# Kernel optimization log

Measured on AMD Instinct MI355X. Metric: run time of the kernel, lower is better.

Reference implementation:

```python
import jax, jax.numpy as jnp
import numpy as np
import math

B, S, HID = 2, 2048, 512
NH, NKV, HD = 8, 2, 256
ROT = 64          # partial_rotary_factor 0.25 * head_dim 256
ROPE_THETA = 10000000.0
EPS = 1e-6


def _rms_norm(x, w):
    # zero-centered RMSNorm: x / rms * (1 + w)
    rms = jnp.sqrt(jnp.mean(x * x, axis=-1, keepdims=True) + EPS)
    return x / rms * (1.0 + w)


def _partial_rope(x, cos, sin):
    # x: [B,S,H,HD]; cos/sin: [S, ROT//2]
    xr = x[..., :ROT].reshape(*x.shape[:-1], ROT // 2, 2)
    a, b = xr[..., 0], xr[..., 1]
    c = cos[None, :, None, :]
    s = sin[None, :, None, :]
    rot = jnp.stack([a * c - b * s, a * s + b * c], axis=-1).reshape(*x.shape[:-1], ROT)
    return jnp.concatenate([rot, x[..., ROT:]], axis=-1)


def setup_inputs() -> dict:
    key = jax.random.key(0)
    ks = jax.random.split(key, 6)
    x = jax.random.normal(ks[0], (B, S, HID), dtype=jnp.float32)
    # real RoPE frequencies
    inv_freq = 1.0 / (ROPE_THETA ** (np.arange(0, ROT, 2, dtype=np.float32) / ROT))
    t = np.arange(S, dtype=np.float32)
    angles = np.outer(t, inv_freq)  # [S, ROT//2]
    cos = jnp.asarray(np.cos(angles), dtype=jnp.float32)
    sin = jnp.asarray(np.sin(angles), dtype=jnp.float32)
    # additive causal mask [S,S]
    mask = jnp.where(jnp.tril(jnp.ones((S, S), dtype=bool)), 0.0, -1e9).astype(jnp.float32)
    sc = 0.02
    wq = jax.random.normal(ks[1], (HID, NH * HD), dtype=jnp.float32) * sc
    wk = jax.random.normal(ks[2], (HID, NKV * HD), dtype=jnp.float32) * sc
    wv = jax.random.normal(ks[3], (HID, NKV * HD), dtype=jnp.float32) * sc
    wo = jax.random.normal(ks[4], (NH * HD, HID), dtype=jnp.float32) * sc
    q_norm_w = jnp.zeros((HD,), dtype=jnp.float32)
    k_norm_w = jnp.zeros((HD,), dtype=jnp.float32)
    return {"x": x, "cos": cos, "sin": sin, "mask": mask,
            "wq": wq, "wk": wk, "wv": wv, "wo": wo,
            "q_norm_w": q_norm_w, "k_norm_w": k_norm_w}


def reference(x, cos, sin, mask, wq, wk, wv, wo, q_norm_w, k_norm_w):
    b, s, _ = x.shape
    groups = NH // NKV
    q = (x @ wq).reshape(b, s, NH, HD)
    k = (x @ wk).reshape(b, s, NKV, HD)
    v = (x @ wv).reshape(b, s, NKV, HD)
    q = _partial_rope(_rms_norm(q, q_norm_w), cos, sin)
    k = _partial_rope(_rms_norm(k, k_norm_w), cos, sin)
    # GQA: broadcast kv heads to NH
    k = jnp.repeat(k, groups, axis=2)  # [b,s,NH,HD]
    v = jnp.repeat(v, groups, axis=2)
    scale = math.sqrt(HD)
    scores = jnp.einsum('bqhd,bkhd->bhqk', q, k) / scale
    scores = scores + mask[None, None, :, :]
    attn = jax.nn.softmax(scores, axis=-1)
    out = jnp.einsum('bhqk,bkhd->bqhd', attn, v).reshape(b, s, NH * HD)
    return out @ wo
```

## Files before the change

kernel.cpp:

```cpp
#include <hip/hip_runtime.h>

#define S_LEN 2048
#define NHQ 8
#define NKV 2
#define HD 256
#define KVB 32

typedef __attribute__((ext_vector_type(8))) short bf16x8;
typedef __attribute__((ext_vector_type(4))) short bf16x4;
typedef __attribute__((ext_vector_type(4))) float f32x4;
typedef __attribute__((ext_vector_type(16))) float f32x16;
typedef __attribute__((ext_vector_type(4))) unsigned u32x4;

__device__ __forceinline__ short f2bf(float f) {
    unsigned u = __builtin_bit_cast(unsigned, f);
    u += 0x7FFFu + ((u >> 16) & 1u);
    return (short)(u >> 16);
}
__device__ __forceinline__ float bf2f(short s) {
    unsigned u = ((unsigned)(unsigned short)s) << 16;
    return __builtin_bit_cast(float, u);
}
__device__ __forceinline__ unsigned cvtpk(float a, float b) {
    unsigned r;
    asm("v_cvt_pk_bf16_f32 %0, %1, %2" : "=v"(r) : "v"(a), "v"(b));
    return r;
}
__device__ __forceinline__ void gload16(const short* g, short* l) {
    __builtin_amdgcn_global_load_lds((const __attribute__((address_space(1))) unsigned*)g,
                                     (__attribute__((address_space(3))) unsigned*)l, 16, 0, 0);
}
__device__ __forceinline__ float bperm(int srclane, float v) {
    return __builtin_bit_cast(float,
        __builtin_amdgcn_ds_bpermute(srclane * 4, __builtin_bit_cast(int, v)));
}

__global__ __launch_bounds__(256) void cvt_kernel(const float* __restrict__ in,
                                                  short* __restrict__ out, int n) {
    int i = (blockIdx.x * 256 + threadIdx.x) * 4;
    if (i + 3 < n) {
        float4 f = *(const float4*)(in + i);
        bf16x4 o;
        o[0] = f2bf(f.x); o[1] = f2bf(f.y); o[2] = f2bf(f.z); o[3] = f2bf(f.w);
        *(bf16x4*)(out + i) = o;
    }
}

__global__ __launch_bounds__(256) void wt_kernel(const float* __restrict__ in,
                                                 short* __restrict__ out,
                                                 int K, int N) {
    __shared__ short tile[64][72];
    int n0 = blockIdx.x * 64, k0 = blockIdx.y * 64;
    int t = threadIdx.x;
    #pragma unroll
    for (int i = 0; i < 16; i++) {
        int flat = i * 256 + t; int r = flat >> 6, c = flat & 63;
        tile[r][c] = f2bf(in[(long)(k0 + r) * N + n0 + c]);
    }
    __syncthreads();
    #pragma unroll
    for (int i = 0; i < 16; i++) {
        int flat = i * 256 + t; int r = flat >> 6, c = flat & 63;
        out[(long)(n0 + r) * K + k0 + c] = tile[c][r];
    }
}

template<int BN, int WRITE_BF16>
__global__ __launch_bounds__(256) void gemm_bt(const short* __restrict__ A,
                                               const short* __restrict__ Bt,
                                               void* __restrict__ Cv,
                                               int M, int N, int K) {
    constexpr int NI = BN / 32;
    __shared__ short As[128 * 32];
    __shared__ short Bs[BN * 32];
    const int t = threadIdx.x;
    const int lane = t & 63, w = t >> 6;
    const int lr = lane & 15, lg = lane >> 4;
    const int m0 = blockIdx.y * 128, n0 = blockIdx.x * BN;
    const int wm = (w >> 1) * 64, wn = (w & 1) * (BN / 2);

    f32x4 acc[4][NI];
    #pragma unroll
    for (int i = 0; i < 4; i++)
        #pragma unroll
        for (int j = 0; j < NI; j++) acc[i][j] = (f32x4){0.f, 0.f, 0.f, 0.f};

    for (int k0 = 0; k0 < K; k0 += 32) {
        __syncthreads();
        #pragma unroll
        for (int r = 0; r < 2; r++) {
            int sbase = r * 2048 + w * 512;
            int srow = (sbase + lane * 8) >> 5, scol = (sbase + lane * 8) & 31;
            gload16(A + (long)(m0 + srow) * K + k0 + scol, &As[sbase]);
        }
        #pragma unroll
        for (int r = 0; r < BN / 64; r++) {
            int sbase = r * 2048 + w * 512;
            int srow = (sbase + lane * 8) >> 5, scol = (sbase + lane * 8) & 31;
            gload16(Bt + (long)(n0 + srow) * K + k0 + scol, &Bs[sbase]);
        }
        __syncthreads();
        bf16x8 af[4], bfr[NI];
        #pragma unroll
        for (int mi = 0; mi < 4; mi++)
            af[mi] = *(const bf16x8*)&As[(wm + mi * 16 + lr) * 32 + lg * 8];
        #pragma unroll
        for (int ni = 0; ni < NI; ni++)
            bfr[ni] = *(const bf16x8*)&Bs[(wn + ni * 16 + lr) * 32 + lg * 8];
        #pragma unroll
        for (int mi = 0; mi < 4; mi++)
            #pragma unroll
            for (int ni = 0; ni < NI; ni++)
                acc[mi][ni] = __builtin_amdgcn_mfma_f32_16x16x32_bf16(af[mi], bfr[ni], acc[mi][ni], 0, 0, 0);
    }
    #pragma unroll
    for (int mi = 0; mi < 4; mi++)
    #pragma unroll
    for (int ni = 0; ni < NI; ni++)
    #pragma unroll
    for (int r = 0; r < 4; r++) {
        long row = m0 + wm + mi * 16 + lg * 4 + r;
        long col = n0 + wn + ni * 16 + lr;
        float v = acc[mi][ni][r];
        if (WRITE_BF16) ((short*)Cv)[row * N + col] = f2bf(v);
        else            ((float*)Cv)[row * N + col] = v;
    }
}

__global__ __launch_bounds__(256) void norm_rope_kernel(
    const short* __restrict__ in, short* __restrict__ out,
    const float* __restrict__ w, const float* __restrict__ cosb,
    const float* __restrict__ sinb, int H, long ldin, long cofs,
    long ob, long oh, long os, float scale) {
    int vec = blockIdx.x * 4 + (threadIdx.x >> 6);
    int lane = threadIdx.x & 63;
    int token = vec / H, head = vec % H;
    int b = token / S_LEN, s = token % S_LEN;

    bf16x4 xv = *(const bf16x4*)(in + (long)token * ldin + cofs + head * 256 + lane * 4);
    float x0 = bf2f(xv[0]), x1 = bf2f(xv[1]), x2 = bf2f(xv[2]), x3 = bf2f(xv[3]);
    float ss = x0 * x0 + x1 * x1 + x2 * x2 + x3 * x3;
    #pragma unroll
    for (int m = 1; m < 64; m <<= 1) ss += __shfl_xor(ss, m);
    float inv = rsqrtf(ss * (1.f / 256.f) + 1e-6f);

    float4 wv = *(const float4*)(w + lane * 4);
    float y0 = x0 * inv * (1.f + wv.x);
    float y1 = x1 * inv * (1.f + wv.y);
    float y2 = x2 * inv * (1.f + wv.z);
    float y3 = x3 * inv * (1.f + wv.w);

    if (lane < 16) {
        float2 c = *(const float2*)&cosb[s * 32 + lane * 2];
        float2 sn = *(const float2*)&sinb[s * 32 + lane * 2];
        float a0 = y0 * c.x - y1 * sn.x, b0 = y0 * sn.x + y1 * c.x;
        float a1 = y2 * c.y - y3 * sn.y, b1 = y2 * sn.y + y3 * c.y;
        y0 = a0; y1 = b0; y2 = a1; y3 = b1;
    }
    y0 *= scale; y1 *= scale; y2 *= scale; y3 *= scale;
    long oidx = (long)b * ob + (long)head * oh + (long)s * os + lane * 4;
    bf16x4 o; o[0] = f2bf(y0); o[1] = f2bf(y1); o[2] = f2bf(y2); o[3] = f2bf(y3);
    *(bf16x4*)(out + oidx) = o;
}

__global__ __launch_bounds__(256) void transpose_v_kernel(const short* __restrict__ C,
                                                          short* __restrict__ vr) {
    __shared__ short tile[64][65];
    int s0 = blockIdx.x * 64, d0 = blockIdx.y * 64;
    int bkv = blockIdx.z; int b = bkv >> 1, kv = bkv & 1;
    int t = threadIdx.x;
    #pragma unroll
    for (int i = 0; i < 16; i++) {
        int flat = i * 256 + t; int si = flat >> 6, di = flat & 63;
        tile[si][di] = C[(long)(b * S_LEN + s0 + si) * 3072 + 2560 + kv * 256 + d0 + di];
    }
    __syncthreads();
    #pragma unroll
    for (int i = 0; i < 16; i++) {
        int flat = i * 256 + t; int di = flat >> 6, si = flat & 63;
        vr[(long)(bkv * 256 + d0 + di) * S_LEN + s0 + si] = tile[si][di];
    }
}

__global__ __launch_bounds__(512, 2) void flash_kernel(const short* __restrict__ Q,
                                                       const short* __restrict__ Kt,
                                                       const short* __restrict__ Vt,
                                                       short* __restrict__ O) {
    __shared__ __align__(16) char smem[132096];

    int idx = blockIdx.x;
    int a = idx >> 4;
    int bh = idx & 15, h = bh & 7, b = bh >> 3;
    int kv = h >> 2;
    int t = threadIdx.x, lane = t & 63, w = t >> 6;
    int g = w >> 1, p = w & 1;
    int ln = lane & 31, hi = lane >> 5;
    int q0 = a * 128 + g * 32;
    int qg = q0 + ln;

    const short* Kb = Kt + (long)(b * NKV + kv) * S_LEN * HD;
    const short* Vb = Vt + (long)(b * NKV + kv) * HD * S_LEN;

    bf16x8 qf[16];
    {
        const short* qrow = Q + ((long)(b * S_LEN + qg) * NHQ + h) * HD + hi * 8;
        #pragma unroll
        for (int dc = 0; dc < 16; dc++) qf[dc] = *(const bf16x8*)&qrow[dc * 16];
    }

    f32x16 acc[8];
    #pragma unroll
    for (int i = 0; i < 8; i++)
        #pragma unroll
        for (int j = 0; j < 16; j++) acc[i][j] = 0.f;
    float m = -1e30f, l = 0.f;

    const int nph  = 2 * a + 2;
    const int Tmax = 4 * a + g;

    auto stagepair = [&](int sp, int T0) {
        #pragma unroll
        for (int pp = 0; pp < 2; pp++) {
            int k0s = (T0 + pp) * KVB;
            short* Ktile = (short*)(smem + (sp * 2 + pp) * 16384);
            short* Vtile = (short*)(smem + 65536 + (sp * 2 + pp) * 16384);
            #pragma unroll
            for (int c = 0; c < 2; c++) {
                int o = c * 8192 + w * 1024 + lane * 16;
                int key = o >> 9, db = o & 511;
                gload16(Kb + (long)(k0s + key) * HD + ((db ^ ((key & 7) << 4)) >> 1),
                        Ktile + (c * 8192 + w * 1024) / 2);
                int d = o >> 6, kb = o & 63;
                gload16(Vb + (long)d * S_LEN + k0s + ((kb ^ ((d & 6) << 3)) >> 1),
                        Vtile + (c * 8192 + w * 1024) / 2);
            }
        }
    };

    auto computeT = [&](int sp, int T) {
        const char* Ks = (const char*)smem + (sp * 2 + p) * 16384;
        const char* Vs = (const char*)smem + 65536 + (sp * 2 + p) * 16384;
        int k0 = T * KVB;
        f32x16 sA, sB;
        #pragma unroll
        for (int j = 0; j < 16; j++) { sA[j] = 0.f; sB[j] = 0.f; }
        __builtin_amdgcn_s_setprio(1);
        #pragma unroll
        for (int dc = 0; dc < 16; dc += 2) {
            int kb0 = (dc * 32 + hi * 16) ^ ((ln & 7) << 4);
            int kb1 = ((dc + 1) * 32 + hi * 16) ^ ((ln & 7) << 4);
            bf16x8 kf0 = *(const bf16x8*)(Ks + ln * 512 + kb0);
            bf16x8 kf1 = *(const bf16x8*)(Ks + ln * 512 + kb1);
            sA = __builtin_amdgcn_mfma_f32_32x32x16_bf16(kf0, qf[dc],     sA, 0, 0, 0);
            sB = __builtin_amdgcn_mfma_f32_32x32x16_bf16(kf1, qf[dc + 1], sB, 0, 0, 0);
        }
        __builtin_amdgcn_s_setprio(0);
        f32x16 s;
        #pragma unroll
        for (int j = 0; j < 16; j++) s[j] = sA[j] + sB[j];

        if (k0 + KVB - 1 > q0) {
            #pragma unroll
            for (int r = 0; r < 16; r++) {
                int key_g = k0 + (r & 3) + 8 * (r >> 2) + 4 * hi;
                if (key_g > qg) s[r] = -1e30f;
            }
        }
        float mt = s[0];
        #pragma unroll
        for (int r = 1; r < 16; r++) mt = fmaxf(mt, s[r]);
        mt = fmaxf(mt, __shfl_xor(mt, 32));
        float mn = m;
        if (!__all(mt <= m + 8.f)) {
            mn = fmaxf(m, mt);
            float f = __expf(m - mn);
            m = mn;
            float fr[16];
            #pragma unroll
            for (int r = 0; r < 16; r++)
                fr[r] = bperm((r & 3) + 8 * (r >> 2) + 4 * hi, f);
            #pragma unroll
            for (int i = 0; i < 8; i++)
                #pragma unroll
                for (int r = 0; r < 16; r++) acc[i][r] *= fr[r];
            l *= f;
        }
        float pr[16], ps = 0.f;
        #pragma unroll
        for (int r = 0; r < 16; r++) { pr[r] = __expf(s[r] - mn); ps += pr[r]; }
        ps += __shfl_xor(ps, 32);
        l += ps;

        unsigned pw[8];
        #pragma unroll
        for (int kc = 0; kc < 2; kc++) {
            unsigned X = cvtpk(pr[kc * 8 + 0], pr[kc * 8 + 1]);
            unsigned Y = cvtpk(pr[kc * 8 + 4], pr[kc * 8 + 5]);
            unsigned Z = cvtpk(pr[kc * 8 + 2], pr[kc * 8 + 3]);
            unsigned W = cvtpk(pr[kc * 8 + 6], pr[kc * 8 + 7]);
            asm volatile("v_permlane32_swap_b32 %0, %1" : "+v"(X), "+v"(Y));
            asm volatile("v_permlane32_swap_b32 %0, %1" : "+v"(Z), "+v"(W));
            pw[kc * 4 + 0] = X; pw[kc * 4 + 1] = Z;
            pw[kc * 4 + 2] = Y; pw[kc * 4 + 3] = W;
        }
        u32x4 w0v = {pw[0], pw[1], pw[2], pw[3]};
        u32x4 w1v = {pw[4], pw[5], pw[6], pw[7]};
        bf16x8 pa0 = __builtin_bit_cast(bf16x8, w0v);
        bf16x8 pa1 = __builtin_bit_cast(bf16x8, w1v);

        __builtin_amdgcn_s_setprio(1);
        #pragma unroll
        for (int db = 0; db < 8; db++) {
            int drow = db * 32 + ln;
            int sw = (drow & 6) << 3;
            bf16x8 vf0 = *(const bf16x8*)(Vs + drow * 64 + ((hi * 16) ^ sw));
            bf16x8 vf1 = *(const bf16x8*)(Vs + drow * 64 + ((32 + hi * 16) ^ sw));
            acc[db] = __builtin_amdgcn_mfma_f32_32x32x16_bf16(pa0, vf0, acc[db], 0, 0, 0);
            acc[db] = __builtin_amdgcn_mfma_f32_32x32x16_bf16(pa1, vf1, acc[db], 0, 0, 0);
        }
        __builtin_amdgcn_s_setprio(0);
    };

    stagepair(0, 0);
    stagepair(1, 2);

    for (int ph = 0; ph < nph; ph++) {
        int sp = ph & 1;
        if (ph + 1 < nph) { asm volatile("s_waitcnt vmcnt(8)" ::: "memory"); }
        else              { asm volatile("s_waitcnt vmcnt(0)" ::: "memory"); }
        __builtin_amdgcn_s_barrier();
        int T = 2 * ph + p;
        if (T <= Tmax) computeT(sp, T);
        __builtin_amdgcn_s_barrier();
        if (ph + 2 < nph) stagepair(sp, 2 * ph + 4);
        __builtin_amdgcn_sched_barrier(0);
    }

    float* accb = (float*)smem;
    float* mlb  = (float*)(smem + 131072);
    if (p == 1) {
        #pragma unroll
        for (int db = 0; db < 8; db++)
            #pragma unroll
            for (int r = 0; r < 16; r++)
                accb[g * 8192 + (db * 16 + r) * 64 + hi * 32 + ln] = acc[db][r];
        if (hi == 0) { mlb[g * 32 + ln] = m; mlb[128 + g * 32 + ln] = l; }
    }
    __syncthreads();
    if (p == 0) {
        float m1 = mlb[g * 32 + ln], l1 = mlb[128 + g * 32 + ln];
        float M  = fmaxf(m, m1);
        float f0 = __expf(m - M), f1 = __expf(m1 - M);
        float lt = l * f0 + l1 * f1;
        float w0 = f0 / lt, w1 = f1 / lt;
        float fr0[16], fr1[16];
        #pragma unroll
        for (int r = 0; r < 16; r++) {
            int crow = (r & 3) + 8 * (r >> 2) + 4 * hi;
            fr0[r] = bperm(crow, w0);
            fr1[r] = bperm(crow, w1);
        }
        #pragma unroll
        for (int db = 0; db < 8; db++)
            #pragma unroll
            for (int r = 0; r < 16; r++) {
                float a1 = accb[g * 8192 + (db * 16 + r) * 64 + hi * 32 + ln];
                int qrow = q0 + (r & 3) + 8 * (r >> 2) + 4 * hi;
                O[(long)(b * S_LEN + qrow) * 2048 + h * HD + db * 32 + ln] =
                    f2bf(acc[db][r] * fr0[r] + a1 * fr1[r]);
            }
    }
}

extern "C" void kernel_launch(void* const* d_in, const int* in_sizes, int n_in,
                              void* d_out, int out_size, void* d_ws, size_t ws_size,
                              hipStream_t stream) {
    const float* x    = (const float*)d_in[0];
    const float* cosb = (const float*)d_in[1];
    const float* sinb = (const float*)d_in[2];
    const float* wq   = (const float*)d_in[4];
    const float* wk   = (const float*)d_in[5];
    const float* wv   = (const float*)d_in[6];
    const float* wo   = (const float*)d_in[7];
    const float* qnw  = (const float*)d_in[8];
    const float* knw  = (const float*)d_in[9];
    float* out = (float*)d_out;

    char* ws = (char*)d_ws;
    short* xb   = (short*)(ws + 0);
    short* wfus = (short*)(ws + 4194304);
    short* wot  = (short*)(ws + 7340032);
    short* C    = (short*)(ws + 9437184);
    short* ao   = (short*)(ws + 9437184);
    short* qro  = (short*)(ws + 34603008);
    short* kr   = (short*)(ws + 51380224);
    short* vr   = (short*)(ws + 55574528);

    cvt_kernel<<<2048, 256, 0, stream>>>(x, xb, 2097152);
    wt_kernel<<<dim3(32, 8), 256, 0, stream>>>(wq, wfus,              512, 2048);
    wt_kernel<<<dim3(8, 8),  256, 0, stream>>>(wk, wfus + 2048 * 512, 512, 512);
    wt_kernel<<<dim3(8, 8),  256, 0, stream>>>(wv, wfus + 2560 * 512, 512, 512);
    wt_kernel<<<dim3(8, 32), 256, 0, stream>>>(wo, wot, 2048, 512);

    gemm_bt<128, 1><<<dim3(24, 32), 256, 0, stream>>>(xb, wfus, C, 4096, 3072, 512);

    norm_rope_kernel<<<8192, 256, 0, stream>>>(C, qro, qnw, cosb, sinb, 8,
                                               3072L, 0L, 4194304L, 256L, 2048L, 0.0625f);
    norm_rope_kernel<<<2048, 256, 0, stream>>>(C, kr, knw, cosb, sinb, 2,
                                               3072L, 2048L, 1048576L, 524288L, 256L, 1.0f);
    transpose_v_kernel<<<dim3(32, 4, 4), 256, 0, stream>>>(C, vr);

    flash_kernel<<<256, 512, 0, stream>>>(qro, kr, vr, ao);

    gemm_bt<64, 0><<<dim3(8, 32), 256, 0, stream>>>(ao, wot, out, 4096, 512, 2048);
}
```

Baseline: 215.6 us.

## Split flash attention into 64-row blocks with XCD-aware longest-first scheduling

The flash kernel now runs 512 blocks of 256 threads, each owning 64 query rows instead of 128, and uses half the shared memory. Block indices are remapped so that each XCD handles two (batch, head) pairs and the largest causal blocks are dispatched first, which targets tail imbalance and L2 locality for K/V. The two-stage double buffer is replaced by a single buffer with a full vmcnt(0) wait each iteration, so load latency is no longer hidden behind compute. In exchange, fewer threads per block and smaller LDS usage should let more blocks reside per CU.

```diff
diff --git a/kernel.cpp b/kernel.cpp
--- a/kernel.cpp
+++ b/kernel.cpp
@@ -182,20 +182,22 @@
     }
 }
 
-__global__ __launch_bounds__(512, 2) void flash_kernel(const short* __restrict__ Q,
+__global__ __launch_bounds__(256, 2) void flash_kernel(const short* __restrict__ Q,
                                                        const short* __restrict__ Kt,
                                                        const short* __restrict__ Vt,
                                                        short* __restrict__ O) {
-    __shared__ __align__(16) char smem[132096];
+    __shared__ __align__(16) char smem[66048];
 
     int idx = blockIdx.x;
-    int a = idx >> 4;
-    int bh = idx & 15, h = bh & 7, b = bh >> 3;
+    int xcd = idx & 7, slot = idx >> 3;
+    int bh = xcd * 2 + (slot & 1);
+    int j  = 31 - (slot >> 1);
+    int h = bh & 7, b = bh >> 3;
     int kv = h >> 2;
     int t = threadIdx.x, lane = t & 63, w = t >> 6;
     int g = w >> 1, p = w & 1;
     int ln = lane & 31, hi = lane >> 5;
-    int q0 = a * 128 + g * 32;
+    int q0 = j * 64 + g * 32;
     int qg = q0 + ln;
 
     const short* Kb = Kt + (long)(b * NKV + kv) * S_LEN * HD;
@@ -212,38 +214,34 @@
     #pragma unroll
     for (int i = 0; i < 8; i++)
         #pragma unroll
-        for (int j = 0; j < 16; j++) acc[i][j] = 0.f;
+        for (int jj = 0; jj < 16; jj++) acc[i][jj] = 0.f;
     float m = -1e30f, l = 0.f;
 
-    const int nph  = 2 * a + 2;
-    const int Tmax = 4 * a + g;
-
-    auto stagepair = [&](int sp, int T0) {
+    auto stage = [&](int ph2) {
         #pragma unroll
         for (int pp = 0; pp < 2; pp++) {
-            int k0s = (T0 + pp) * KVB;
-            short* Ktile = (short*)(smem + (sp * 2 + pp) * 16384);
-            short* Vtile = (short*)(smem + 65536 + (sp * 2 + pp) * 16384);
-            #pragma unroll
-            for (int c = 0; c < 2; c++) {
-                int o = c * 8192 + w * 1024 + lane * 16;
+            int k0s = (2 * ph2 + pp) * KVB;
+            short* Ktile = (short*)(smem + pp * 16384);
+            short* Vtile = (short*)(smem + 32768 + pp * 16384);
+            #pragma unroll
+            for (int c = 0; c < 4; c++) {
+                int o = c * 4096 + w * 1024 + lane * 16;
                 int key = o >> 9, db = o & 511;
                 gload16(Kb + (long)(k0s + key) * HD + ((db ^ ((key & 7) << 4)) >> 1),
-                        Ktile + (c * 8192 + w * 1024) / 2);
+                        Ktile + (c * 4096 + w * 1024) / 2);
                 int d = o >> 6, kb = o & 63;
                 gload16(Vb + (long)d * S_LEN + k0s + ((kb ^ ((d & 6) << 3)) >> 1),
-                        Vtile + (c * 8192 + w * 1024) / 2);
+                        Vtile + (c * 4096 + w * 1024) / 2);
             }
         }
     };
 
-    auto computeT = [&](int sp, int T) {
-        const char* Ks = (const char*)smem + (sp * 2 + p) * 16384;
-        const char* Vs = (const char*)smem + 65536 + (sp * 2 + p) * 16384;
-        int k0 = T * KVB;
+    auto compute = [&](int k0) {
+        const char* Ks = (const char*)smem + p * 16384;
+        const char* Vs = (const char*)smem + 32768 + p * 16384;
         f32x16 sA, sB;
         #pragma unroll
-        for (int j = 0; j < 16; j++) { sA[j] = 0.f; sB[j] = 0.f; }
+        for (int r = 0; r < 16; r++) { sA[r] = 0.f; sB[r] = 0.f; }
         __builtin_amdgcn_s_setprio(1);
         #pragma unroll
         for (int dc = 0; dc < 16; dc += 2) {
@@ -257,7 +255,7 @@
         __builtin_amdgcn_s_setprio(0);
         f32x16 s;
         #pragma unroll
-        for (int j = 0; j < 16; j++) s[j] = sA[j] + sB[j];
+        for (int r = 0; r < 16; r++) s[r] = sA[r] + sB[r];
 
         if (k0 + KVB - 1 > q0) {
             #pragma unroll
@@ -321,34 +319,30 @@
         __builtin_amdgcn_s_setprio(0);
     };
 
-    stagepair(0, 0);
-    stagepair(1, 2);
-
-    for (int ph = 0; ph < nph; ph++) {
-        int sp = ph & 1;
-        if (ph + 1 < nph) { asm volatile("s_waitcnt vmcnt(8)" ::: "memory"); }
-        else              { asm volatile("s_waitcnt vmcnt(0)" ::: "memory"); }
+    stage(0);
+    for (int ph = 0; ph <= j; ph++) {
+        asm volatile("s_waitcnt vmcnt(0)" ::: "memory");
         __builtin_amdgcn_s_barrier();
-        int T = 2 * ph + p;
-        if (T <= Tmax) computeT(sp, T);
+        int k0 = (2 * ph + p) * KVB;
+        if (k0 <= q0 + 31) compute(k0);
         __builtin_amdgcn_s_barrier();
-        if (ph + 2 < nph) stagepair(sp, 2 * ph + 4);
+        if (ph < j) stage(ph + 1);
         __builtin_amdgcn_sched_barrier(0);
     }
 
     float* accb = (float*)smem;
-    float* mlb  = (float*)(smem + 131072);
+    float* mlb  = (float*)(smem + 65536);
     if (p == 1) {
         #pragma unroll
         for (int db = 0; db < 8; db++)
             #pragma unroll
             for (int r = 0; r < 16; r++)
                 accb[g * 8192 + (db * 16 + r) * 64 + hi * 32 + ln] = acc[db][r];
-        if (hi == 0) { mlb[g * 32 + ln] = m; mlb[128 + g * 32 + ln] = l; }
+        if (hi == 0) { mlb[g * 32 + ln] = m; mlb[64 + g * 32 + ln] = l; }
     }
     __syncthreads();
     if (p == 0) {
-        float m1 = mlb[g * 32 + ln], l1 = mlb[128 + g * 32 + ln];
+        float m1 = mlb[g * 32 + ln], l1 = mlb[64 + g * 32 + ln];
         float M  = fmaxf(m, m1);
         float f0 = __expf(m - M), f1 = __expf(m1 - M);
         float lt = l * f0 + l1 * f1;
@@ -410,7 +404,7 @@
                                                3072L, 2048L, 1048576L, 524288L, 256L, 1.0f);
     transpose_v_kernel<<<dim3(32, 4, 4), 256, 0, stream>>>(C, vr);
 
-    flash_kernel<<<256, 512, 0, stream>>>(qro, kr, vr, ao);
+    flash_kernel<<<512, 256, 0, stream>>>(qro, kr, vr, ao);
 
     gemm_bt<64, 0><<<dim3(8, 32), 256, 0, stream>>>(ao, wot, out, 4096, 512, 2048);
 }
```

New measurement: 199.9 us. 7.3% less time.
